# Optimization experiments

Hardware: AMD Instinct MI355X
Metric: run time of the kernel (lower is better)

## Reference

```python
import jax, jax.numpy as jnp
import numpy as np
from jax import lax

B, H, N, D = 8, 8, 4096, 64
NUM_LANDMARKS = 256
PINV_ITERS = 6
KERNEL = 33


def moore_penrose_iter_pinv(x, iters=PINV_ITERS):
    # x: [b, h, m, m]
    abs_x = jnp.abs(x)
    col = abs_x.sum(axis=-1)
    row = abs_x.sum(axis=-2)
    z = jnp.swapaxes(x, -1, -2) / (jnp.max(col) * jnp.max(row))
    I = jnp.eye(x.shape[-1], dtype=x.dtype)
    for _ in range(iters):
        xz = x @ z
        z = 0.25 * z @ (13.0 * I - xz @ (15.0 * I - xz @ (7.0 * I - xz)))
    return z


def setup_inputs() -> dict:
    key = jax.random.key(0)
    ks = jax.random.split(key, 10)
    inp = {
        'q': jax.random.normal(ks[0], (B, H, N, D), dtype=jnp.float32),
        'k': jax.random.normal(ks[1], (B, H, N, D), dtype=jnp.float32),
        'v': jax.random.normal(ks[2], (B, H, N, D), dtype=jnp.float32),
        'Wsim1': jax.random.uniform(ks[3], (H, H), dtype=jnp.float32),
        'Wsim2': jax.random.uniform(ks[4], (H, H), dtype=jnp.float32),
        'Wsim3': jax.random.uniform(ks[5], (H, H), dtype=jnp.float32),
        'Wattn1': jax.random.uniform(ks[6], (H, H), dtype=jnp.float32),
        'Wattn2': jax.random.uniform(ks[7], (H, H), dtype=jnp.float32),
        'Wattn3': jax.random.uniform(ks[8], (H, H), dtype=jnp.float32),
        'conv_w': jax.random.normal(ks[9], (H, H, KERNEL, 1), dtype=jnp.float32) * 0.05,
    }
    return inp


def reference(q, k, v, Wsim1, Wsim2, Wsim3, Wattn1, Wattn2, Wattn3, conv_w):
    b, h, n, d = q.shape
    # m = max(12, min(num_landmarks, int((sqrt(kn) + sqrt(qn)) // 2))) -> 64 for n=4096
    m = max(12, min(NUM_LANDMARKS, int((n ** 0.5 + n ** 0.5) // 2)))
    l = -(-n // m)  # ceil(n / m); n % m == 0 here so no padding branch

    # landmarks: group-sum over l consecutive tokens, divided by l
    q_l = q.reshape(b, h, m, l, d).sum(axis=3) / l  # [b,h,m,d]
    k_l = k.reshape(b, h, m, l, d).sum(axis=3) / l  # [b,h,m,d]

    sim1 = jnp.einsum('bhid,bhjd->bhij', q, k_l)    # [b,h,n,m]
    sim2 = jnp.einsum('bhid,bhjd->bhij', q_l, k_l)  # [b,h,m,m]
    sim3 = jnp.einsum('bhid,bhjd->bhij', q_l, k)    # [b,h,m,n]

    # talking-head mixing on sims
    sim1 = jnp.einsum('bhij,hk->bkij', sim1, Wsim1)
    sim2 = jnp.einsum('bhij,hk->bkij', sim2, Wsim2)
    sim3 = jnp.einsum('bhij,hk->bkij', sim3, Wsim3)

    attn1 = jax.nn.softmax(sim1, axis=-1)
    attn2 = jax.nn.softmax(sim2, axis=-1)
    attn3 = jax.nn.softmax(sim3, axis=-1)

    attn2_inv = moore_penrose_iter_pinv(attn2, PINV_ITERS)

    # talking-head mixing on attns
    attn1 = jnp.einsum('bhij,hk->bkij', attn1, Wattn1)
    attn2_inv = jnp.einsum('bhij,hk->bkij', attn2_inv, Wattn2)
    attn3 = jnp.einsum('bhij,hk->bkij', attn3, Wattn3)

    out = attn1 @ (attn2_inv @ (attn3 @ v))  # [b,h,n,d]

    # residual depthwise-ish conv over (n, d) treating heads as channels
    pad = KERNEL // 2
    res = lax.conv_general_dilated(
        v, conv_w,
        window_strides=(1, 1),
        padding=[(pad, pad), (0, 0)],
        dimension_numbers=('NCHW', 'OIHW', 'NCHW'))
    out = out + res
    return out
```

## Files before the change

### kernel.cpp

```cpp
#include <hip/hip_runtime.h>
#include <cstddef>
#include <cstdint>

constexpr int cB = 8, cH = 8, cN = 4096, cD = 64, cM = 64, cL = 64;

__global__ void k_landmarks(const float* __restrict__ q, const float* __restrict__ k,
                            float* __restrict__ ql, float* __restrict__ kl) {
  int bm = blockIdx.x;
  int bh = bm >> 6, m = bm & 63;
  int d = threadIdx.x;
  size_t base = ((size_t)bh * cN + (size_t)m * cL) * cD + d;
  float sq = 0.f, sk = 0.f;
  for (int t = 0; t < cL; ++t) {
    sq += q[base + (size_t)t * cD];
    sk += k[base + (size_t)t * cD];
  }
  size_t ob = ((size_t)bh * cM + m) * cD + d;
  ql[ob] = sq * (1.0f / cL);
  kl[ob] = sk * (1.0f / cL);
}

__global__ void __launch_bounds__(256) k_sim2(const float* __restrict__ ql,
                                              const float* __restrict__ kl,
                                              const float* __restrict__ Wsim2,
                                              float* __restrict__ attn2,
                                              unsigned int* __restrict__ scal,
                                              float* __restrict__ klT) {
  __shared__ float qs[64][65];
  __shared__ float ks[64][65];
  __shared__ float acc[64 * 65];
  int b = blockIdx.x >> 3, kk = blockIdx.x & 7;
  int tid = threadIdx.x;
  for (int idx = tid; idx < 64 * 64; idx += 256)
    acc[(idx >> 6) * 65 + (idx & 63)] = 0.f;
  int ri = (tid >> 4) * 4, ci = (tid & 15) * 4;
  for (int h = 0; h < 8; ++h) {
    __syncthreads();
    const float* qg = ql + (size_t)(b * 8 + h) * 4096;
    const float* kg = kl + (size_t)(b * 8 + h) * 4096;
    for (int idx = tid; idx < 4096; idx += 256) {
      qs[idx >> 6][idx & 63] = qg[idx];
      ks[idx >> 6][idx & 63] = kg[idx];
    }
    __syncthreads();
    if (h == kk) {
      float* op = klT + (size_t)(b * 8 + kk) * 4096;
      for (int idx = tid; idx < 4096; idx += 256)
        op[idx] = ks[idx & 63][idx >> 6];
    }
    float w = Wsim2[h * 8 + kk];
    float s[4][4] = {};
    for (int d = 0; d < 64; ++d) {
      float a0 = qs[ri][d], a1 = qs[ri + 1][d], a2 = qs[ri + 2][d], a3 = qs[ri + 3][d];
      float b0 = ks[ci][d], b1 = ks[ci + 1][d], b2 = ks[ci + 2][d], b3 = ks[ci + 3][d];
      s[0][0] += a0 * b0; s[0][1] += a0 * b1; s[0][2] += a0 * b2; s[0][3] += a0 * b3;
      s[1][0] += a1 * b0; s[1][1] += a1 * b1; s[1][2] += a1 * b2; s[1][3] += a1 * b3;
      s[2][0] += a2 * b0; s[2][1] += a2 * b1; s[2][2] += a2 * b2; s[2][3] += a2 * b3;
      s[3][0] += a3 * b0; s[3][1] += a3 * b1; s[3][2] += a3 * b2; s[3][3] += a3 * b3;
    }
    #pragma unroll
    for (int x = 0; x < 4; ++x)
      #pragma unroll
      for (int y = 0; y < 4; ++y)
        acc[(ri + x) * 65 + ci + y] += w * s[x][y];
  }
  __syncthreads();
  if (tid < 64) {
    float mx = -1e30f;
    for (int j = 0; j < 64; ++j) mx = fmaxf(mx, acc[tid * 65 + j]);
    float s = 0.f;
    for (int j = 0; j < 64; ++j) {
      float e = expf(acc[tid * 65 + j] - mx);
      acc[tid * 65 + j] = e;
      s += e;
    }
    float inv = 1.0f / s;
    float rs = 0.f;
    for (int j = 0; j < 64; ++j) {
      float p = acc[tid * 65 + j] * inv;
      acc[tid * 65 + j] = p;
      rs += p;
    }
    atomicMax(scal + 1, __float_as_uint(rs));
  }
  __syncthreads();
  if (tid < 64) {
    float cs = 0.f;
    for (int i = 0; i < 64; ++i) cs += acc[i * 65 + tid];
    atomicMax(scal + 0, __float_as_uint(cs));
  }
  __syncthreads();
  float* op = attn2 + (size_t)(b * 8 + kk) * 4096;
  for (int idx = tid; idx < 4096; idx += 256)
    op[idx] = acc[(idx >> 6) * 65 + (idx & 63)];
}

__device__ __forceinline__ void mm64(float* __restrict__ Dst, const float* S,
                                     float c0, float c1, const float* __restrict__ P,
                                     const float* __restrict__ Q, int tid) {
  int ri = (tid >> 4) * 4, ci = (tid & 15) * 4;
  float s[4][4] = {};
  for (int k = 0; k < 64; ++k) {
    float a0 = P[(ri + 0) * 65 + k], a1 = P[(ri + 1) * 65 + k];
    float a2 = P[(ri + 2) * 65 + k], a3 = P[(ri + 3) * 65 + k];
    float b0 = Q[k * 65 + ci + 0], b1 = Q[k * 65 + ci + 1];
    float b2 = Q[k * 65 + ci + 2], b3 = Q[k * 65 + ci + 3];
    s[0][0] += a0 * b0; s[0][1] += a0 * b1; s[0][2] += a0 * b2; s[0][3] += a0 * b3;
    s[1][0] += a1 * b0; s[1][1] += a1 * b1; s[1][2] += a1 * b2; s[1][3] += a1 * b3;
    s[2][0] += a2 * b0; s[2][1] += a2 * b1; s[2][2] += a2 * b2; s[2][3] += a2 * b3;
    s[3][0] += a3 * b0; s[3][1] += a3 * b1; s[3][2] += a3 * b2; s[3][3] += a3 * b3;
  }
  #pragma unroll
  for (int x = 0; x < 4; ++x)
    #pragma unroll
    for (int y = 0; y < 4; ++y) {
      float r = c1 * s[x][y];
      if (S) r += c0 * S[(ri + x) * 65 + ci + y];
      Dst[(ri + x) * 65 + ci + y] = r;
    }
}

__global__ void __launch_bounds__(256) k_pinv(const float* __restrict__ attn2,
                                              float* __restrict__ attn2inv,
                                              const unsigned int* __restrict__ scal) {
  __shared__ float bufs[5][64 * 65];
  float* X = bufs[0];
  float* Z = bufs[1];
  float* T1 = bufs[2];
  float* T2 = bufs[3];
  float* T3 = bufs[4];
  int tid = threadIdx.x;
  const float* xg = attn2 + (size_t)blockIdx.x * 4096;
  for (int idx = tid; idx < 4096; idx += 256)
    X[(idx >> 6) * 65 + (idx & 63)] = xg[idx];
  float denom = __uint_as_float(scal[0]) * __uint_as_float(scal[1]);
  float invd = 1.0f / denom;
  __syncthreads();
  for (int idx = tid; idx < 4096; idx += 256) {
    int i = idx >> 6, j = idx & 63;
    Z[i * 65 + j] = X[j * 65 + i] * invd;
  }
  __syncthreads();
  for (int it = 0; it < 6; ++it) {
    mm64(T1, nullptr, 0.f, 1.f, X, Z, tid);          __syncthreads();
    mm64(T2, T1, 7.f, -1.f, T1, T1, tid);            __syncthreads();
    mm64(T3, T1, 15.f, -1.f, T1, T2, tid);           __syncthreads();
    mm64(T2, Z, 13.f * 0.25f, -0.25f, Z, T3, tid);   __syncthreads();
    float* tmp = Z; Z = T2; T2 = tmp;
  }
  float* og = attn2inv + (size_t)blockIdx.x * 4096;
  for (int idx = tid; idx < 4096; idx += 256)
    og[idx] = Z[(idx >> 6) * 65 + (idx & 63)];
}

__global__ void __launch_bounds__(512) k_sim3(const float* __restrict__ ql,
                                              const float* __restrict__ kg,
                                              const float* __restrict__ Wsim3,
                                              float* __restrict__ sim3m) {
  __shared__ float qls[64 * 65];
  __shared__ float ksT[64 * 36];
  __shared__ float w3[64];
  int b = blockIdx.x >> 7, jt = blockIdx.x & 127;
  int j0 = jt * 32, tid = threadIdx.x;
  if (tid < 64) w3[tid] = Wsim3[tid];
  int i = tid >> 3, jb = (tid & 7) * 4;
  float acc[8][4] = {};
  for (int h = 0; h < 8; ++h) {
    __syncthreads();
    const float* qg = ql + (size_t)(b * 8 + h) * 4096;
    for (int idx = tid; idx < 4096; idx += 512)
      qls[(idx >> 6) * 65 + (idx & 63)] = qg[idx];
    const float* kp = kg + ((size_t)(b * 8 + h) * cN + j0) * 64;
    for (int idx = tid; idx < 2048; idx += 512) {
      int j = idx >> 6, d = idx & 63;
      ksT[d * 36 + j] = kp[idx];
    }
    __syncthreads();
    float s[4] = {};
    for (int d = 0; d < 64; ++d) {
      float a = qls[i * 65 + d];
      float4 kv = *(const float4*)&ksT[d * 36 + jb];
      s[0] += a * kv.x; s[1] += a * kv.y; s[2] += a * kv.z; s[3] += a * kv.w;
    }
    #pragma unroll
    for (int k = 0; k < 8; ++k) {
      float w = w3[h * 8 + k];
      #pragma unroll
      for (int c = 0; c < 4; ++c) acc[k][c] += w * s[c];
    }
  }
  #pragma unroll
  for (int k = 0; k < 8; ++k) {
    float* op = sim3m + ((size_t)((b * 8 + k) * 64 + i)) * cN + j0 + jb;
    *(float4*)op = make_float4(acc[k][0], acc[k][1], acc[k][2], acc[k][3]);
  }
}

__global__ void __launch_bounds__(512) k_smxt3(float* __restrict__ sim3m,
                                               const float* __restrict__ Wattn3) {
  __shared__ float S[8][4096];
  __shared__ float w[64];
  __shared__ float red[8];
  int b = blockIdx.x >> 6, i = blockIdx.x & 63;
  int tid = threadIdx.x;
  if (tid < 64) w[tid] = Wattn3[tid];
  float m[8], inv[8];
  for (int k = 0; k < 8; ++k) {
    float* rp = sim3m + ((size_t)((b * 8 + k) * 64 + i)) * cN;
    float vv[8];
    float mx = -1e30f;
    #pragma unroll
    for (int t = 0; t < 8; ++t) {
      vv[t] = rp[tid + t * 512];
      S[k][tid + t * 512] = vv[t];
      mx = fmaxf(mx, vv[t]);
    }
    for (int off = 32; off > 0; off >>= 1) mx = fmaxf(mx, __shfl_down(mx, off));
    __syncthreads();
    if ((tid & 63) == 0) red[tid >> 6] = mx;
    __syncthreads();
    mx = fmaxf(fmaxf(fmaxf(red[0], red[1]), fmaxf(red[2], red[3])),
               fmaxf(fmaxf(red[4], red[5]), fmaxf(red[6], red[7])));
    float s = 0.f;
    #pragma unroll
    for (int t = 0; t < 8; ++t) s += expf(vv[t] - mx);
    for (int off = 32; off > 0; off >>= 1) s += __shfl_down(s, off);
    __syncthreads();
    if ((tid & 63) == 0) red[tid >> 6] = s;
    __syncthreads();
    float st = red[0] + red[1] + red[2] + red[3] +
               red[4] + red[5] + red[6] + red[7];
    m[k] = mx;
    inv[k] = 1.0f / st;
  }
  __syncthreads();
  for (int j = tid; j < 4096; j += 512) {
    float p[8];
    #pragma unroll
    for (int k = 0; k < 8; ++k) p[k] = expf(S[k][j] - m[k]) * inv[k];
    #pragma unroll
    for (int k2 = 0; k2 < 8; ++k2) {
      float t = 0.f;
      #pragma unroll
      for (int k = 0; k < 8; ++k) t += p[k] * w[k * 8 + k2];
      sim3m[((size_t)((b * 8 + k2) * 64 + i)) * cN + j] = t;
    }
  }
}

__global__ void __launch_bounds__(256) k_t3(const float* __restrict__ attn3f,
                                            const float* __restrict__ v,
                                            float* __restrict__ T3p) {
  __shared__ float As[64][65];
  __shared__ float Vs[64][68];
  int bh = blockIdx.x >> 2, chunk = blockIdx.x & 3;
  int tid = threadIdx.x;
  int ri = (tid >> 4) * 4, ci = (tid & 15) * 4;
  float acc[4][4] = {};
  for (int jt = chunk * 16; jt < chunk * 16 + 16; ++jt) {
    __syncthreads();
    const float* ap = attn3f + (size_t)bh * 64 * cN + jt * 64;
    for (int idx = tid; idx < 4096; idx += 256)
      As[idx >> 6][idx & 63] = ap[(size_t)(idx >> 6) * cN + (idx & 63)];
    const float* vp = v + ((size_t)bh * cN + jt * 64) * 64;
    for (int idx = tid; idx < 4096; idx += 256)
      Vs[idx >> 6][idx & 63] = vp[idx];
    __syncthreads();
    for (int j = 0; j < 64; ++j) {
      float a0 = As[ri][j], a1 = As[ri + 1][j], a2 = As[ri + 2][j], a3 = As[ri + 3][j];
      float b0 = Vs[j][ci], b1 = Vs[j][ci + 1], b2 = Vs[j][ci + 2], b3 = Vs[j][ci + 3];
      acc[0][0] += a0 * b0; acc[0][1] += a0 * b1; acc[0][2] += a0 * b2; acc[0][3] += a0 * b3;
      acc[1][0] += a1 * b0; acc[1][1] += a1 * b1; acc[1][2] += a1 * b2; acc[1][3] += a1 * b3;
      acc[2][0] += a2 * b0; acc[2][1] += a2 * b1; acc[2][2] += a2 * b2; acc[2][3] += a2 * b3;
      acc[3][0] += a3 * b0; acc[3][1] += a3 * b1; acc[3][2] += a3 * b2; acc[3][3] += a3 * b3;
    }
  }
  float* op = T3p + ((size_t)chunk * 64 + bh) * 4096;
  #pragma unroll
  for (int x = 0; x < 4; ++x)
    #pragma unroll
    for (int y = 0; y < 4; ++y)
      op[(ri + x) * 64 + ci + y] = acc[x][y];
}

__global__ void __launch_bounds__(256) k_t2(const float* __restrict__ attn2inv,
                                            const float* __restrict__ Wattn2,
                                            const float* __restrict__ T3p,
                                            float* __restrict__ T2) {
  __shared__ float As[64][65];
  __shared__ float Bs[64][68];
  __shared__ float w2[8];
  int bh = blockIdx.x, tid = threadIdx.x;
  int b = bh >> 3, h = bh & 7;
  if (tid < 8) w2[tid] = Wattn2[tid * 8 + h];
  __syncthreads();
  const float* ib = attn2inv + (size_t)b * 8 * 4096;
  for (int idx = tid; idx < 4096; idx += 256) {
    float s = 0.f;
    #pragma unroll
    for (int k = 0; k < 8; ++k) s += ib[(size_t)k * 4096 + idx] * w2[k];
    As[idx >> 6][idx & 63] = s;
    float t = 0.f;
    #pragma unroll
    for (int c = 0; c < 4; ++c) t += T3p[((size_t)c * 64 + bh) * 4096 + idx];
    Bs[idx >> 6][idx & 63] = t;
  }
  __syncthreads();
  int ri = (tid >> 4) * 4, ci = (tid & 15) * 4;
  float acc[4][4] = {};
  for (int j = 0; j < 64; ++j) {
    float a0 = As[ri][j], a1 = As[ri + 1][j], a2 = As[ri + 2][j], a3 = As[ri + 3][j];
    float b0 = Bs[j][ci], b1 = Bs[j][ci + 1], b2 = Bs[j][ci + 2], b3 = Bs[j][ci + 3];
    acc[0][0] += a0 * b0; acc[0][1] += a0 * b1; acc[0][2] += a0 * b2; acc[0][3] += a0 * b3;
    acc[1][0] += a1 * b0; acc[1][1] += a1 * b1; acc[1][2] += a1 * b2; acc[1][3] += a1 * b3;
    acc[2][0] += a2 * b0; acc[2][1] += a2 * b1; acc[2][2] += a2 * b2; acc[2][3] += a2 * b3;
    acc[3][0] += a3 * b0; acc[3][1] += a3 * b1; acc[3][2] += a3 * b2; acc[3][3] += a3 * b3;
  }
  #pragma unroll
  for (int x = 0; x < 4; ++x)
    #pragma unroll
    for (int y = 0; y < 4; ++y)
      T2[(size_t)bh * 4096 + (ri + x) * 64 + ci + y] = acc[x][y];
}

__global__ void __launch_bounds__(256) k_conv(const float* __restrict__ v,
                                              const float* __restrict__ cw,
                                              float* __restrict__ out) {
  __shared__ float wl[2112];
  int tid = threadIdx.x;
  for (int idx = tid; idx < 2112; idx += 256) {
    int o = idx / 264, r = idx % 264, i = r / 33, t = r % 33;
    wl[i * 264 + t * 8 + o] = cw[idx];
  }
  __syncthreads();
  int d = tid & 63;
  int sub = tid >> 6;
  int b = blockIdx.x >> 7;
  int n0 = (blockIdx.x & 127) * 32 + sub * 8;
  int lo = n0 - 16;
  bool interior = (lo >= 0) && (lo + 39 < cN);
  float acc[8][8] = {};
  for (int i = 0; i < 8; ++i) {
    const float* vp = v + ((size_t)(b * 8 + i) * cN) * 64 + d;
    float win[40];
    if (interior) {
      #pragma unroll
      for (int t = 0; t < 40; ++t) win[t] = vp[(size_t)(lo + t) * 64];
    } else {
      #pragma unroll
      for (int t = 0; t < 40; ++t) {
        int nn = lo + t;
        win[t] = (nn >= 0 && nn < cN) ? vp[(size_t)nn * 64] : 0.f;
      }
    }
    #pragma unroll
    for (int t = 0; t < 33; ++t) {
      float4 w0 = *(const float4*)&wl[i * 264 + t * 8];
      float4 w1 = *(const float4*)&wl[i * 264 + t * 8 + 4];
      #pragma unroll
      for (int u = 0; u < 8; ++u) {
        float val = win[t + u];
        acc[0][u] += val * w0.x; acc[1][u] += val * w0.y;
        acc[2][u] += val * w0.z; acc[3][u] += val * w0.w;
        acc[4][u] += val * w1.x; acc[5][u] += val * w1.y;
        acc[6][u] += val * w1.z; acc[7][u] += val * w1.w;
      }
    }
  }
  #pragma unroll
  for (int o = 0; o < 8; ++o) {
    float* op = out + ((size_t)(b * 8 + o) * cN + n0) * 64 + d;
    #pragma unroll
    for (int u = 0; u < 8; ++u) op[(size_t)u * 64] = acc[o][u];
  }
}

__device__ __forceinline__ void dot64_4x4(const float* __restrict__ A,
                                          const float* __restrict__ Bm, int jb,
                                          float s[4][4]) {
  #pragma unroll
  for (int dc = 0; dc < 16; ++dc) {
    float4 kv0 = *(const float4*)&Bm[(dc * 4 + 0) * 68 + jb];
    float4 kv1 = *(const float4*)&Bm[(dc * 4 + 1) * 68 + jb];
    float4 kv2 = *(const float4*)&Bm[(dc * 4 + 2) * 68 + jb];
    float4 kv3 = *(const float4*)&Bm[(dc * 4 + 3) * 68 + jb];
    #pragma unroll
    for (int r = 0; r < 4; ++r) {
      float4 af = *(const float4*)&A[r * 68 + dc * 4];
      s[r][0] += af.x * kv0.x; s[r][1] += af.x * kv0.y; s[r][2] += af.x * kv0.z; s[r][3] += af.x * kv0.w;
      s[r][0] += af.y * kv1.x; s[r][1] += af.y * kv1.y; s[r][2] += af.y * kv1.z; s[r][3] += af.y * kv1.w;
      s[r][0] += af.z * kv2.x; s[r][1] += af.z * kv2.y; s[r][2] += af.z * kv2.z; s[r][3] += af.z * kv2.w;
      s[r][0] += af.w * kv3.x; s[r][1] += af.w * kv3.y; s[r][2] += af.w * kv3.z; s[r][3] += af.w * kv3.w;
    }
  }
}

__device__ __forceinline__ void stage_q(float* __restrict__ dst,
                                        const float4* __restrict__ src, int tid) {
  int sr = tid >> 4, sc = (tid & 15) * 4;
  float4 a = src[tid];
  float4 b = src[tid + 512];
  float4 c = src[tid + 1024];
  float4 d = src[tid + 1536];
  *(float4*)&dst[sr * 68 + sc] = a;
  *(float4*)&dst[(32 + sr) * 68 + sc] = b;
  *(float4*)&dst[(64 + sr) * 68 + sc] = c;
  *(float4*)&dst[(96 + sr) * 68 + sc] = d;
}

__device__ __forceinline__ void stage_l(float* __restrict__ dst,
                                        const float4* __restrict__ src, int tid) {
  int sr = tid >> 4, sc = (tid & 15) * 4;
  float4 a = src[tid];
  float4 b = src[tid + 512];
  *(float4*)&dst[sr * 68 + sc] = a;
  *(float4*)&dst[(32 + sr) * 68 + sc] = b;
}

__global__ void __launch_bounds__(512) k_final(const float* __restrict__ q,
                                               const float* __restrict__ klT,
                                               const float* __restrict__ T2,
                                               const float* __restrict__ Wsim1,
                                               const float* __restrict__ Wattn1,
                                               float* __restrict__ out) {
  __shared__ float SB[2 * 128 * 68 + 2 * 64 * 68];
  __shared__ float ws1[64], wa1[64];
  constexpr int PITCH = 68, QBUF = 128 * 68, LBUF = 64 * 68;
  float* Q0 = SB;
  float* L0 = SB + 2 * QBUF;
  int b = blockIdx.x >> 5, i0 = (blockIdx.x & 31) * 128;
  int tid = threadIdx.x;
  if (tid < 64) { ws1[tid] = Wsim1[tid]; wa1[tid] = Wattn1[tid]; }
  int jb = (tid & 15) * 4, r0 = (tid >> 4) * 4;

  float sim[8][4][4] = {};

  const float4* qb = (const float4*)(q + ((size_t)(b * 8) * cN + i0) * 64);
  const float4* kb = (const float4*)(klT + (size_t)(b * 8) * 4096);
  const float4* tb = (const float4*)(T2 + (size_t)(b * 8) * 4096);

  stage_q(Q0, qb, tid);
  stage_l(L0, kb, tid);
  __syncthreads();

  for (int h = 0; h < 7; ++h) {
    int p = h & 1, pn = p ^ 1;
    stage_q(Q0 + pn * QBUF, qb + (size_t)(h + 1) * 65536, tid);
    stage_l(L0 + pn * LBUF, kb + (size_t)(h + 1) * 1024, tid);
    float s[4][4] = {};
    dot64_4x4(Q0 + p * QBUF + r0 * PITCH, L0 + p * LBUF, jb, s);
    #pragma unroll
    for (int kq = 0; kq < 8; ++kq) {
      float wv = ws1[h * 8 + kq];
      #pragma unroll
      for (int r = 0; r < 4; ++r)
        #pragma unroll
        for (int c = 0; c < 4; ++c) sim[kq][r][c] += wv * s[r][c];
    }
    __syncthreads();
  }

  {
    stage_l(L0, tb, tid);
    float s[4][4] = {};
    dot64_4x4(Q0 + 1 * QBUF + r0 * PITCH, L0 + 1 * LBUF, jb, s);
    #pragma unroll
    for (int kq = 0; kq < 8; ++kq) {
      float wv = ws1[56 + kq];
      #pragma unroll
      for (int r = 0; r < 4; ++r)
        #pragma unroll
        for (int c = 0; c < 4; ++c) sim[kq][r][c] += wv * s[r][c];
    }
    #pragma unroll
    for (int kq = 0; kq < 8; ++kq) {
      #pragma unroll
      for (int r = 0; r < 4; ++r) {
        float mx = fmaxf(fmaxf(sim[kq][r][0], sim[kq][r][1]),
                         fmaxf(sim[kq][r][2], sim[kq][r][3]));
        mx = fmaxf(mx, __shfl_xor(mx, 1)); mx = fmaxf(mx, __shfl_xor(mx, 2));
        mx = fmaxf(mx, __shfl_xor(mx, 4)); mx = fmaxf(mx, __shfl_xor(mx, 8));
        float sm = 0.f;
        #pragma unroll
        for (int c = 0; c < 4; ++c) {
          sim[kq][r][c] = expf(sim[kq][r][c] - mx);
          sm += sim[kq][r][c];
        }
        sm += __shfl_xor(sm, 1); sm += __shfl_xor(sm, 2);
        sm += __shfl_xor(sm, 4); sm += __shfl_xor(sm, 8);
        float inv = 1.0f / sm;
        #pragma unroll
        for (int c = 0; c < 4; ++c) sim[kq][r][c] *= inv;
      }
    }
    #pragma unroll
    for (int r = 0; r < 4; ++r)
      #pragma unroll
      for (int c = 0; c < 4; ++c) {
        float t[8];
        #pragma unroll
        for (int k2 = 0; k2 < 8; ++k2) {
          float a = 0.f;
          #pragma unroll
          for (int kk = 0; kk < 8; ++kk) a += sim[kk][r][c] * wa1[kk * 8 + k2];
          t[k2] = a;
        }
        #pragma unroll
        for (int k2 = 0; k2 < 8; ++k2) sim[k2][r][c] = t[k2];
      }
    #pragma unroll
    for (int r = 0; r < 4; ++r)
      *(float4*)&Q0[(r0 + r) * PITCH + jb] =
          make_float4(sim[0][r][0], sim[0][r][1], sim[0][r][2], sim[0][r][3]);
    __syncthreads();
  }

  #pragma unroll
  for (int k2 = 0; k2 < 8; ++k2) {
    int p = k2 & 1, pn = p ^ 1;
    if (k2 < 7) {
      stage_l(L0 + pn * LBUF, tb + (size_t)(k2 + 1) * 1024, tid);
      #pragma unroll
      for (int r = 0; r < 4; ++r)
        *(float4*)&Q0[pn * QBUF + (r0 + r) * PITCH + jb] =
            make_float4(sim[k2 + 1][r][0], sim[k2 + 1][r][1],
                        sim[k2 + 1][r][2], sim[k2 + 1][r][3]);
    }
    float o[4][4] = {};
    dot64_4x4(Q0 + p * QBUF + r0 * PITCH, L0 + p * LBUF, jb, o);
    #pragma unroll
    for (int r = 0; r < 4; ++r) {
      float* op = out + ((size_t)(b * 8 + k2) * cN + i0 + r0 + r) * 64 + jb;
      float4 e = *(float4*)op;
      e.x += o[r][0]; e.y += o[r][1]; e.z += o[r][2]; e.w += o[r][3];
      *(float4*)op = e;
    }
    if (k2 < 7) __syncthreads();
  }
}

extern "C" void kernel_launch(void* const* d_in, const int* in_sizes, int n_in,
                              void* d_out, int out_size, void* d_ws, size_t ws_size,
                              hipStream_t stream) {
  const float* q = (const float*)d_in[0];
  const float* k = (const float*)d_in[1];
  const float* v = (const float*)d_in[2];
  const float* Wsim1 = (const float*)d_in[3];
  const float* Wsim2 = (const float*)d_in[4];
  const float* Wsim3 = (const float*)d_in[5];
  const float* Wattn1 = (const float*)d_in[6];
  const float* Wattn2 = (const float*)d_in[7];
  const float* Wattn3 = (const float*)d_in[8];
  const float* cw = (const float*)d_in[9];
  float* out = (float*)d_out;
  float* ws = (float*)d_ws;

  float* ql       = ws + 0;
  float* kl       = ws + 262144;
  float* attn2    = ws + 524288;
  float* attn2inv = ws + 786432;
  float* klT      = ws + 1048576;
  float* T2       = ws + 1310720;
  unsigned int* scal = (unsigned int*)(ws + 1581056);
  float* T3p      = ws + 1581120;
  float* sim3m = out;

  hipMemsetAsync(scal, 0, 8, stream);
  k_landmarks<<<dim3(4096), dim3(64), 0, stream>>>(q, k, ql, kl);
  k_sim2<<<dim3(64), dim3(256), 0, stream>>>(ql, kl, Wsim2, attn2, scal, klT);
  k_pinv<<<dim3(64), dim3(256), 0, stream>>>(attn2, attn2inv, scal);
  k_sim3<<<dim3(1024), dim3(512), 0, stream>>>(ql, k, Wsim3, sim3m);
  k_smxt3<<<dim3(512), dim3(512), 0, stream>>>(sim3m, Wattn3);
  k_t3<<<dim3(256), dim3(256), 0, stream>>>(sim3m, v, T3p);
  k_t2<<<dim3(64), dim3(256), 0, stream>>>(attn2inv, Wattn2, T3p, T2);
  k_conv<<<dim3(1024), dim3(256), 0, stream>>>(v, cw, out);
  k_final<<<dim3(256), dim3(512), 0, stream>>>(q, klT, T2, Wsim1, Wattn1, out);
}
```

Before: 805.4 us.

## Vectorize shared-memory GEMM loads with float4 and enlarge k_sim3 tile

Changes the shared-memory padding from 65 to 68 floats so rows are 16-byte aligned, which lets the small 64x64 GEMM inner loops in sim2, pinv, t3 and t2 read operands with float4 loads. k_sim3 is retiled so each block covers 128 key columns and each thread computes a 4x4 output tile instead of 1x4. This raises reuse of the landmark queries and keys and cuts the block count from 1024 to 256. The cost is a larger per-thread accumulator in k_sim3 (128 floats), which raises register pressure and lowers occupancy, and the stride-68 layout may bring back some bank conflicts.

```diff
diff --git a/kernel.cpp b/kernel.cpp
--- a/kernel.cpp
+++ b/kernel.cpp
@@ -26,8 +26,8 @@
                                               float* __restrict__ attn2,
                                               unsigned int* __restrict__ scal,
                                               float* __restrict__ klT) {
-  __shared__ float qs[64][65];
-  __shared__ float ks[64][65];
+  __shared__ float qs[64 * 68];
+  __shared__ float ks[64 * 68];
   __shared__ float acc[64 * 65];
   int b = blockIdx.x >> 3, kk = blockIdx.x & 7;
   int tid = threadIdx.x;
@@ -39,24 +39,42 @@
     const float* qg = ql + (size_t)(b * 8 + h) * 4096;
     const float* kg = kl + (size_t)(b * 8 + h) * 4096;
     for (int idx = tid; idx < 4096; idx += 256) {
-      qs[idx >> 6][idx & 63] = qg[idx];
-      ks[idx >> 6][idx & 63] = kg[idx];
+      qs[(idx >> 6) * 68 + (idx & 63)] = qg[idx];
+      ks[(idx >> 6) * 68 + (idx & 63)] = kg[idx];
     }
     __syncthreads();
     if (h == kk) {
       float* op = klT + (size_t)(b * 8 + kk) * 4096;
       for (int idx = tid; idx < 4096; idx += 256)
-        op[idx] = ks[idx & 63][idx >> 6];
+        op[idx] = ks[(idx & 63) * 68 + (idx >> 6)];
     }
     float w = Wsim2[h * 8 + kk];
     float s[4][4] = {};
-    for (int d = 0; d < 64; ++d) {
-      float a0 = qs[ri][d], a1 = qs[ri + 1][d], a2 = qs[ri + 2][d], a3 = qs[ri + 3][d];
-      float b0 = ks[ci][d], b1 = ks[ci + 1][d], b2 = ks[ci + 2][d], b3 = ks[ci + 3][d];
-      s[0][0] += a0 * b0; s[0][1] += a0 * b1; s[0][2] += a0 * b2; s[0][3] += a0 * b3;
-      s[1][0] += a1 * b0; s[1][1] += a1 * b1; s[1][2] += a1 * b2; s[1][3] += a1 * b3;
-      s[2][0] += a2 * b0; s[2][1] += a2 * b1; s[2][2] += a2 * b2; s[2][3] += a2 * b3;
-      s[3][0] += a3 * b0; s[3][1] += a3 * b1; s[3][2] += a3 * b2; s[3][3] += a3 * b3;
+    for (int dc = 0; dc < 16; ++dc) {
+      float4 qa0 = *(const float4*)&qs[(ri + 0) * 68 + dc * 4];
+      float4 qa1 = *(const float4*)&qs[(ri + 1) * 68 + dc * 4];
+      float4 qa2 = *(const float4*)&qs[(ri + 2) * 68 + dc * 4];
+      float4 qa3 = *(const float4*)&qs[(ri + 3) * 68 + dc * 4];
+      float4 kb0 = *(const float4*)&ks[(ci + 0) * 68 + dc * 4];
+      float4 kb1 = *(const float4*)&ks[(ci + 1) * 68 + dc * 4];
+      float4 kb2 = *(const float4*)&ks[(ci + 2) * 68 + dc * 4];
+      float4 kb3 = *(const float4*)&ks[(ci + 3) * 68 + dc * 4];
+      s[0][0] += qa0.x*kb0.x + qa0.y*kb0.y + qa0.z*kb0.z + qa0.w*kb0.w;
+      s[0][1] += qa0.x*kb1.x + qa0.y*kb1.y + qa0.z*kb1.z + qa0.w*kb1.w;
+      s[0][2] += qa0.x*kb2.x + qa0.y*kb2.y + qa0.z*kb2.z + qa0.w*kb2.w;
+      s[0][3] += qa0.x*kb3.x + qa0.y*kb3.y + qa0.z*kb3.z + qa0.w*kb3.w;
+      s[1][0] += qa1.x*kb0.x + qa1.y*kb0.y + qa1.z*kb0.z + qa1.w*kb0.w;
+      s[1][1] += qa1.x*kb1.x + qa1.y*kb1.y + qa1.z*kb1.z + qa1.w*kb1.w;
+      s[1][2] += qa1.x*kb2.x + qa1.y*kb2.y + qa1.z*kb2.z + qa1.w*kb2.w;
+      s[1][3] += qa1.x*kb3.x + qa1.y*kb3.y + qa1.z*kb3.z + qa1.w*kb3.w;
+      s[2][0] += qa2.x*kb0.x + qa2.y*kb0.y + qa2.z*kb0.z + qa2.w*kb0.w;
+      s[2][1] += qa2.x*kb1.x + qa2.y*kb1.y + qa2.z*kb1.z + qa2.w*kb1.w;
+      s[2][2] += qa2.x*kb2.x + qa2.y*kb2.y + qa2.z*kb2.z + qa2.w*kb2.w;
+      s[2][3] += qa2.x*kb3.x + qa2.y*kb3.y + qa2.z*kb3.z + qa2.w*kb3.w;
+      s[3][0] += qa3.x*kb0.x + qa3.y*kb0.y + qa3.z*kb0.z + qa3.w*kb0.w;
+      s[3][1] += qa3.x*kb1.x + qa3.y*kb1.y + qa3.z*kb1.z + qa3.w*kb1.w;
+      s[3][2] += qa3.x*kb2.x + qa3.y*kb2.y + qa3.z*kb2.z + qa3.w*kb2.w;
+      s[3][3] += qa3.x*kb3.x + qa3.y*kb3.y + qa3.z*kb3.z + qa3.w*kb3.w;
     }
     #pragma unroll
     for (int x = 0; x < 4; ++x)
@@ -100,30 +118,46 @@
                                      const float* __restrict__ Q, int tid) {
   int ri = (tid >> 4) * 4, ci = (tid & 15) * 4;
   float s[4][4] = {};
-  for (int k = 0; k < 64; ++k) {
-    float a0 = P[(ri + 0) * 65 + k], a1 = P[(ri + 1) * 65 + k];
-    float a2 = P[(ri + 2) * 65 + k], a3 = P[(ri + 3) * 65 + k];
-    float b0 = Q[k * 65 + ci + 0], b1 = Q[k * 65 + ci + 1];
-    float b2 = Q[k * 65 + ci + 2], b3 = Q[k * 65 + ci + 3];
-    s[0][0] += a0 * b0; s[0][1] += a0 * b1; s[0][2] += a0 * b2; s[0][3] += a0 * b3;
-    s[1][0] += a1 * b0; s[1][1] += a1 * b1; s[1][2] += a1 * b2; s[1][3] += a1 * b3;
-    s[2][0] += a2 * b0; s[2][1] += a2 * b1; s[2][2] += a2 * b2; s[2][3] += a2 * b3;
-    s[3][0] += a3 * b0; s[3][1] += a3 * b1; s[3][2] += a3 * b2; s[3][3] += a3 * b3;
+  for (int kc = 0; kc < 16; ++kc) {
+    float4 a0 = *(const float4*)&P[(ri + 0) * 68 + kc * 4];
+    float4 a1 = *(const float4*)&P[(ri + 1) * 68 + kc * 4];
+    float4 a2 = *(const float4*)&P[(ri + 2) * 68 + kc * 4];
+    float4 a3 = *(const float4*)&P[(ri + 3) * 68 + kc * 4];
+    float4 b0 = *(const float4*)&Q[(kc * 4 + 0) * 68 + ci];
+    float4 b1 = *(const float4*)&Q[(kc * 4 + 1) * 68 + ci];
+    float4 b2 = *(const float4*)&Q[(kc * 4 + 2) * 68 + ci];
+    float4 b3 = *(const float4*)&Q[(kc * 4 + 3) * 68 + ci];
+    s[0][0] += a0.x*b0.x + a0.y*b1.x + a0.z*b2.x + a0.w*b3.x;
+    s[0][1] += a0.x*b0.y + a0.y*b1.y + a0.z*b2.y + a0.w*b3.y;
+    s[0][2] += a0.x*b0.z + a0.y*b1.z + a0.z*b2.z + a0.w*b3.z;
+    s[0][3] += a0.x*b0.w + a0.y*b1.w + a0.z*b2.w + a0.w*b3.w;
+    s[1][0] += a1.x*b0.x + a1.y*b1.x + a1.z*b2.x + a1.w*b3.x;
+    s[1][1] += a1.x*b0.y + a1.y*b1.y + a1.z*b2.y + a1.w*b3.y;
+    s[1][2] += a1.x*b0.z + a1.y*b1.z + a1.z*b2.z + a1.w*b3.z;
+    s[1][3] += a1.x*b0.w + a1.y*b1.w + a1.z*b2.w + a1.w*b3.w;
+    s[2][0] += a2.x*b0.x + a2.y*b1.x + a2.z*b2.x + a2.w*b3.x;
+    s[2][1] += a2.x*b0.y + a2.y*b1.y + a2.z*b2.y + a2.w*b3.y;
+    s[2][2] += a2.x*b0.z + a2.y*b1.z + a2.z*b2.z + a2.w*b3.z;
+    s[2][3] += a2.x*b0.w + a2.y*b1.w + a2.z*b2.w + a2.w*b3.w;
+    s[3][0] += a3.x*b0.x + a3.y*b1.x + a3.z*b2.x + a3.w*b3.x;
+    s[3][1] += a3.x*b0.y + a3.y*b1.y + a3.z*b2.y + a3.w*b3.y;
+    s[3][2] += a3.x*b0.z + a3.y*b1.z + a3.z*b2.z + a3.w*b3.z;
+    s[3][3] += a3.x*b0.w + a3.y*b1.w + a3.z*b2.w + a3.w*b3.w;
   }
   #pragma unroll
   for (int x = 0; x < 4; ++x)
     #pragma unroll
     for (int y = 0; y < 4; ++y) {
       float r = c1 * s[x][y];
-      if (S) r += c0 * S[(ri + x) * 65 + ci + y];
-      Dst[(ri + x) * 65 + ci + y] = r;
+      if (S) r += c0 * S[(ri + x) * 68 + ci + y];
+      Dst[(ri + x) * 68 + ci + y] = r;
     }
 }
 
 __global__ void __launch_bounds__(256) k_pinv(const float* __restrict__ attn2,
                                               float* __restrict__ attn2inv,
                                               const unsigned int* __restrict__ scal) {
-  __shared__ float bufs[5][64 * 65];
+  __shared__ float bufs[5][64 * 68];
   float* X = bufs[0];
   float* Z = bufs[1];
   float* T1 = bufs[2];
@@ -132,13 +166,13 @@
   int tid = threadIdx.x;
   const float* xg = attn2 + (size_t)blockIdx.x * 4096;
   for (int idx = tid; idx < 4096; idx += 256)
-    X[(idx >> 6) * 65 + (idx & 63)] = xg[idx];
+    X[(idx >> 6) * 68 + (idx & 63)] = xg[idx];
   float denom = __uint_as_float(scal[0]) * __uint_as_float(scal[1]);
   float invd = 1.0f / denom;
   __syncthreads();
   for (int idx = tid; idx < 4096; idx += 256) {
     int i = idx >> 6, j = idx & 63;
-    Z[i * 65 + j] = X[j * 65 + i] * invd;
+    Z[i * 68 + j] = X[j * 68 + i] * invd;
   }
   __syncthreads();
   for (int it = 0; it < 6; ++it) {
@@ -150,50 +184,64 @@
   }
   float* og = attn2inv + (size_t)blockIdx.x * 4096;
   for (int idx = tid; idx < 4096; idx += 256)
-    og[idx] = Z[(idx >> 6) * 65 + (idx & 63)];
+    og[idx] = Z[(idx >> 6) * 68 + (idx & 63)];
 }
 
 __global__ void __launch_bounds__(512) k_sim3(const float* __restrict__ ql,
                                               const float* __restrict__ kg,
                                               const float* __restrict__ Wsim3,
                                               float* __restrict__ sim3m) {
-  __shared__ float qls[64 * 65];
-  __shared__ float ksT[64 * 36];
+  __shared__ float qls[64 * 68];
+  __shared__ float ksT[64 * 132];
   __shared__ float w3[64];
-  int b = blockIdx.x >> 7, jt = blockIdx.x & 127;
-  int j0 = jt * 32, tid = threadIdx.x;
+  int b = blockIdx.x >> 5, jt = blockIdx.x & 31;
+  int j0 = jt * 128, tid = threadIdx.x;
   if (tid < 64) w3[tid] = Wsim3[tid];
-  int i = tid >> 3, jb = (tid & 7) * 4;
-  float acc[8][4] = {};
+  int i0t = (tid >> 5) * 4;
+  int jb = (tid & 31) * 4;
+  float acc[8][4][4] = {};
   for (int h = 0; h < 8; ++h) {
     __syncthreads();
     const float* qg = ql + (size_t)(b * 8 + h) * 4096;
     for (int idx = tid; idx < 4096; idx += 512)
-      qls[(idx >> 6) * 65 + (idx & 63)] = qg[idx];
+      qls[(idx >> 6) * 68 + (idx & 63)] = qg[idx];
     const float* kp = kg + ((size_t)(b * 8 + h) * cN + j0) * 64;
-    for (int idx = tid; idx < 2048; idx += 512) {
+    for (int idx = tid; idx < 8192; idx += 512) {
       int j = idx >> 6, d = idx & 63;
-      ksT[d * 36 + j] = kp[idx];
-    }
-    __syncthreads();
-    float s[4] = {};
-    for (int d = 0; d < 64; ++d) {
-      float a = qls[i * 65 + d];
-      float4 kv = *(const float4*)&ksT[d * 36 + jb];
-      s[0] += a * kv.x; s[1] += a * kv.y; s[2] += a * kv.z; s[3] += a * kv.w;
+      ksT[d * 132 + j] = kp[idx];
+    }
+    __syncthreads();
+    float s[4][4] = {};
+    for (int dc = 0; dc < 16; ++dc) {
+      float4 kv0 = *(const float4*)&ksT[(dc * 4 + 0) * 132 + jb];
+      float4 kv1 = *(const float4*)&ksT[(dc * 4 + 1) * 132 + jb];
+      float4 kv2 = *(const float4*)&ksT[(dc * 4 + 2) * 132 + jb];
+      float4 kv3 = *(const float4*)&ksT[(dc * 4 + 3) * 132 + jb];
+      #pragma unroll
+      for (int r = 0; r < 4; ++r) {
+        float4 af = *(const float4*)&qls[(i0t + r) * 68 + dc * 4];
+        s[r][0] += af.x*kv0.x + af.y*kv1.x + af.z*kv2.x + af.w*kv3.x;
+        s[r][1] += af.x*kv0.y + af.y*kv1.y + af.z*kv2.y + af.w*kv3.y;
+        s[r][2] += af.x*kv0.z + af.y*kv1.z + af.z*kv2.z + af.w*kv3.z;
+        s[r][3] += af.x*kv0.w + af.y*kv1.w + af.z*kv2.w + af.w*kv3.w;
+      }
     }
     #pragma unroll
     for (int k = 0; k < 8; ++k) {
       float w = w3[h * 8 + k];
       #pragma unroll
-      for (int c = 0; c < 4; ++c) acc[k][c] += w * s[c];
+      for (int r = 0; r < 4; ++r)
+        #pragma unroll
+        for (int c = 0; c < 4; ++c) acc[k][r][c] += w * s[r][c];
     }
   }
   #pragma unroll
-  for (int k = 0; k < 8; ++k) {
-    float* op = sim3m + ((size_t)((b * 8 + k) * 64 + i)) * cN + j0 + jb;
-    *(float4*)op = make_float4(acc[k][0], acc[k][1], acc[k][2], acc[k][3]);
-  }
+  for (int k = 0; k < 8; ++k)
+    #pragma unroll
+    for (int r = 0; r < 4; ++r) {
+      float* op = sim3m + ((size_t)((b * 8 + k) * 64 + i0t + r)) * cN + j0 + jb;
+      *(float4*)op = make_float4(acc[k][r][0], acc[k][r][1], acc[k][r][2], acc[k][r][3]);
+    }
 }
 
 __global__ void __launch_bounds__(512) k_smxt3(float* __restrict__ sim3m,
@@ -251,8 +299,8 @@
 __global__ void __launch_bounds__(256) k_t3(const float* __restrict__ attn3f,
                                             const float* __restrict__ v,
                                             float* __restrict__ T3p) {
-  __shared__ float As[64][65];
-  __shared__ float Vs[64][68];
+  __shared__ float As[64 * 68];
+  __shared__ float Vs[64 * 68];
   int bh = blockIdx.x >> 2, chunk = blockIdx.x & 3;
   int tid = threadIdx.x;
   int ri = (tid >> 4) * 4, ci = (tid & 15) * 4;
@@ -261,18 +309,24 @@
     __syncthreads();
     const float* ap = attn3f + (size_t)bh * 64 * cN + jt * 64;
     for (int idx = tid; idx < 4096; idx += 256)
-      As[idx >> 6][idx & 63] = ap[(size_t)(idx >> 6) * cN + (idx & 63)];
+      As[(idx >> 6) * 68 + (idx & 63)] = ap[(size_t)(idx >> 6) * cN + (idx & 63)];
     const float* vp = v + ((size_t)bh * cN + jt * 64) * 64;
     for (int idx = tid; idx < 4096; idx += 256)
-      Vs[idx >> 6][idx & 63] = vp[idx];
-    __syncthreads();
-    for (int j = 0; j < 64; ++j) {
-      float a0 = As[ri][j], a1 = As[ri + 1][j], a2 = As[ri + 2][j], a3 = As[ri + 3][j];
-      float b0 = Vs[j][ci], b1 = Vs[j][ci + 1], b2 = Vs[j][ci + 2], b3 = Vs[j][ci + 3];
-      acc[0][0] += a0 * b0; acc[0][1] += a0 * b1; acc[0][2] += a0 * b2; acc[0][3] += a0 * b3;
-      acc[1][0] += a1 * b0; acc[1][1] += a1 * b1; acc[1][2] += a1 * b2; acc[1][3] += a1 * b3;
-      acc[2][0] += a2 * b0; acc[2][1] += a2 * b1; acc[2][2] += a2 * b2; acc[2][3] += a2 * b3;
-      acc[3][0] += a3 * b0; acc[3][1] += a3 * b1; acc[3][2] += a3 * b2; acc[3][3] += a3 * b3;
+      Vs[(idx >> 6) * 68 + (idx & 63)] = vp[idx];
+    __syncthreads();
+    for (int jc = 0; jc < 16; ++jc) {
+      float4 b0 = *(const float4*)&Vs[(jc * 4 + 0) * 68 + ci];
+      float4 b1 = *(const float4*)&Vs[(jc * 4 + 1) * 68 + ci];
+      float4 b2 = *(const float4*)&Vs[(jc * 4 + 2) * 68 + ci];
+      float4 b3 = *(const float4*)&Vs[(jc * 4 + 3) * 68 + ci];
+      #pragma unroll
+      for (int r = 0; r < 4; ++r) {
+        float4 a = *(const float4*)&As[(ri + r) * 68 + jc * 4];
+        acc[r][0] += a.x*b0.x + a.y*b1.x + a.z*b2.x + a.w*b3.x;
+        acc[r][1] += a.x*b0.y + a.y*b1.y + a.z*b2.y + a.w*b3.y;
+        acc[r][2] += a.x*b0.z + a.y*b1.z + a.z*b2.z + a.w*b3.z;
+        acc[r][3] += a.x*b0.w + a.y*b1.w + a.z*b2.w + a.w*b3.w;
+      }
     }
   }
   float* op = T3p + ((size_t)chunk * 64 + bh) * 4096;
@@ -287,8 +341,8 @@
                                             const float* __restrict__ Wattn2,
                                             const float* __restrict__ T3p,
                                             float* __restrict__ T2) {
-  __shared__ float As[64][65];
-  __shared__ float Bs[64][68];
+  __shared__ float As[64 * 68];
+  __shared__ float Bs[64 * 68];
   __shared__ float w2[8];
   int bh = blockIdx.x, tid = threadIdx.x;
   int b = bh >> 3, h = bh & 7;
@@ -299,22 +353,28 @@
     float s = 0.f;
     #pragma unroll
     for (int k = 0; k < 8; ++k) s += ib[(size_t)k * 4096 + idx] * w2[k];
-    As[idx >> 6][idx & 63] = s;
+    As[(idx >> 6) * 68 + (idx & 63)] = s;
     float t = 0.f;
     #pragma unroll
     for (int c = 0; c < 4; ++c) t += T3p[((size_t)c * 64 + bh) * 4096 + idx];
-    Bs[idx >> 6][idx & 63] = t;
+    Bs[(idx >> 6) * 68 + (idx & 63)] = t;
   }
   __syncthreads();
   int ri = (tid >> 4) * 4, ci = (tid & 15) * 4;
   float acc[4][4] = {};
-  for (int j = 0; j < 64; ++j) {
-    float a0 = As[ri][j], a1 = As[ri + 1][j], a2 = As[ri + 2][j], a3 = As[ri + 3][j];
-    float b0 = Bs[j][ci], b1 = Bs[j][ci + 1], b2 = Bs[j][ci + 2], b3 = Bs[j][ci + 3];
-    acc[0][0] += a0 * b0; acc[0][1] += a0 * b1; acc[0][2] += a0 * b2; acc[0][3] += a0 * b3;
-    acc[1][0] += a1 * b0; acc[1][1] += a1 * b1; acc[1][2] += a1 * b2; acc[1][3] += a1 * b3;
-    acc[2][0] += a2 * b0; acc[2][1] += a2 * b1; acc[2][2] += a2 * b2; acc[2][3] += a2 * b3;
-    acc[3][0] += a3 * b0; acc[3][1] += a3 * b1; acc[3][2] += a3 * b2; acc[3][3] += a3 * b3;
+  for (int jc = 0; jc < 16; ++jc) {
+    float4 b0 = *(const float4*)&Bs[(jc * 4 + 0) * 68 + ci];
+    float4 b1 = *(const float4*)&Bs[(jc * 4 + 1) * 68 + ci];
+    float4 b2 = *(const float4*)&Bs[(jc * 4 + 2) * 68 + ci];
+    float4 b3 = *(const float4*)&Bs[(jc * 4 + 3) * 68 + ci];
+    #pragma unroll
+    for (int r = 0; r < 4; ++r) {
+      float4 a = *(const float4*)&As[(ri + r) * 68 + jc * 4];
+      acc[r][0] += a.x*b0.x + a.y*b1.x + a.z*b2.x + a.w*b3.x;
+      acc[r][1] += a.x*b0.y + a.y*b1.y + a.z*b2.y + a.w*b3.y;
+      acc[r][2] += a.x*b0.z + a.y*b1.z + a.z*b2.z + a.w*b3.z;
+      acc[r][3] += a.x*b0.w + a.y*b1.w + a.z*b2.w + a.w*b3.w;
+    }
   }
   #pragma unroll
   for (int x = 0; x < 4; ++x)
@@ -569,7 +629,7 @@
   k_landmarks<<<dim3(4096), dim3(64), 0, stream>>>(q, k, ql, kl);
   k_sim2<<<dim3(64), dim3(256), 0, stream>>>(ql, kl, Wsim2, attn2, scal, klT);
   k_pinv<<<dim3(64), dim3(256), 0, stream>>>(attn2, attn2inv, scal);
-  k_sim3<<<dim3(1024), dim3(512), 0, stream>>>(ql, k, Wsim3, sim3m);
+  k_sim3<<<dim3(256), dim3(512), 0, stream>>>(ql, k, Wsim3, sim3m);
   k_smxt3<<<dim3(512), dim3(512), 0, stream>>>(sim3m, Wattn3);
   k_t3<<<dim3(256), dim3(256), 0, stream>>>(sim3m, v, T3p);
   k_t2<<<dim3(64), dim3(256), 0, stream>>>(attn2inv, Wattn2, T3p, T2);
```

Result: slower. 924.6 us (+14.8%).
